# Optimization experiments

Measured on AMD Instinct MI355X. Metric: run time of the kernel, lower is better.

The kernel has to match this reference:

```python
import jax, jax.numpy as jnp
import numpy as np

N_NODES = 4096
N_EDGES = 32768
PE_DIM = 16
HIDDEN = 128


def setup_inputs() -> dict:
    key = jax.random.key(0)
    k_nodes, k_send, k_recv, k_w = jax.random.split(key, 4)
    nodes = jax.random.normal(k_nodes, (N_NODES, 8), dtype=jnp.float32)
    senders = jax.random.randint(k_send, (N_EDGES,), 0, N_NODES)
    receivers = jax.random.randint(k_recv, (N_EDGES,), 0, N_NODES)
    W = jax.random.normal(k_w, (PE_DIM, HIDDEN), dtype=jnp.float32) / np.sqrt(PE_DIM).astype(np.float32)
    b = jnp.zeros((HIDDEN,), dtype=jnp.float32)
    return {"nodes": nodes, "senders": senders, "receivers": receivers, "W": W, "b": b}


def reference(nodes, senders, receivers, W, b):
    n = nodes.shape[0]
    pe_dim = W.shape[0]
    # out-degree per node (clamped at 1, as in the original)
    ones = jnp.ones(senders.shape[0], dtype=jnp.float32)
    degree = jnp.maximum(jax.ops.segment_sum(ones, senders, num_segments=n), 1.0)
    inv_deg_e = (1.0 / degree)[senders]  # [E], per-edge 1/deg(sender)

    prob = jnp.eye(n, dtype=jnp.float32)  # [n, n] landing probabilities
    diags = []
    for _ in range(pe_dim):
        # gather sender rows, normalize, scatter-add into receiver rows
        msg = prob[senders] * inv_deg_e[:, None]           # [E, n]
        prob = jax.ops.segment_sum(msg, receivers, num_segments=n)  # [n, n]
        diags.append(jnp.diagonal(prob))                    # return probability A^k_ii
    pe = jnp.stack(diags, axis=-1)  # [n, pe_dim]
    return pe @ W + b               # [n, hidden]
```

## Files before the change

### kernel.cpp

```cpp
#include <hip/hip_runtime.h>

#define NN 4096
#define NE 32768
#define PED 16
#define HID 128
#define CW 16
#define NCHUNK 64
#define THREADS 1024
#define PASSES 4

typedef _Float16 h_t;
typedef _Float16 h8 __attribute__((ext_vector_type(8)));

__device__ __forceinline__ int xbyte(int s) {
  int g = ((s & 3) << 1) | ((s >> 2) & 1);
  return ((s >> 2) << 7) + (g << 4);
}


__global__ void count_kernel(const int* __restrict__ senders,
                             const int* __restrict__ receivers,
                             int* __restrict__ outdeg, int* __restrict__ indeg) {
  int e = blockIdx.x * blockDim.x + threadIdx.x;
  if (e < NE) {
    atomicAdd(&outdeg[senders[e]], 1);
    atomicAdd(&indeg[receivers[e]], 1);
  }
}

__global__ void sort_kernel(const int* __restrict__ indeg, const int* __restrict__ outdeg,
                            float* __restrict__ dinv,
                            int* __restrict__ rowperm, int* __restrict__ sortpos,
                            int* __restrict__ chunk_off, int* __restrict__ chunk_max) {
  __shared__ int hist[64];
  __shared__ int base[64];
  int t = threadIdx.x;
  if (t < 64) hist[t] = 0;
  __syncthreads();
  for (int r = t; r < NN; r += 256) {
    int d = indeg[r]; if (d > 63) d = 63;
    atomicAdd(&hist[d], 1);
    int od = outdeg[r]; if (od < 1) od = 1;
    dinv[r] = 1.0f / (float)od;
  }
  __syncthreads();
  if (t == 0) {
    int acc = 0;
    for (int i = 0; i < 64; ++i) { base[i] = acc; acc += hist[i]; }
  }
  __syncthreads();
  for (int r = t; r < NN; r += 256) {
    int d = indeg[r]; if (d > 63) d = 63;
    int pos = atomicAdd(&base[d], 1);
    rowperm[pos] = r;
    sortpos[r] = pos;
  }
  __syncthreads();
  if (t < NCHUNK) {
    int m = 0;
    for (int i = 0; i < 64; ++i) {
      int d = indeg[rowperm[(t << 6) + i]];
      if (d > m) m = d;
    }
    chunk_max[t] = m;
  }
  __syncthreads();
  if (t == 0) {
    int acc = 0;
    for (int c = 0; c < NCHUNK; ++c) { chunk_off[c] = acc; acc += chunk_max[c] << 6; }
    chunk_off[NCHUNK] = acc;
  }
}

__global__ void zero_tail(const int* __restrict__ chunk_off, int2* __restrict__ e2) {
  int total = chunk_off[NCHUNK];
  e2[total + threadIdx.x] = make_int2(0, 0);
}

__global__ void fill_ell(const int* __restrict__ senders, const int* __restrict__ receivers,
                         const int* __restrict__ sortpos, const int* __restrict__ chunk_off,
                         const float* __restrict__ dinv, int* __restrict__ fillc,
                         int2* __restrict__ ell) {
  int e = blockIdx.x * blockDim.x + threadIdx.x;
  if (e < NE) {
    int r = receivers[e], s = senders[e];
    int p = sortpos[r];
    int tslot = atomicAdd(&fillc[r], 1);
    int slot = chunk_off[p >> 6] + (tslot << 6) + (p & 63);
    ell[slot] = make_int2(xbyte(s), __float_as_int(dinv[s]));
  }
}

__global__ void sched_ell(const int* __restrict__ chunk_off,
                          const int* __restrict__ chunk_max,
                          const int* __restrict__ rowperm,
                          const int* __restrict__ indeg,
                          const int2* __restrict__ src, int2* __restrict__ dst) {
  int p = blockIdx.x * blockDim.x + threadIdx.x;
  int c = p >> 6, l = p & 63;
  int base = chunk_off[c], maxd = chunk_max[c];
  int d = indeg[rowperm[p]];
  if (maxd > 63) {
    for (int t = 0; t < d; ++t) dst[base + (t << 6) + l] = src[base + (t << 6) + l];
    for (int t = d; t < maxd; ++t)
      dst[base + (t << 6) + l] = make_int2(((t + l) & 7) << 4, 0);
    return;
  }
  unsigned long long occ = 0;
  int placed[8] = {0, 0, 0, 0, 0, 0, 0, 0};
  for (int t = 0; t < d; ++t) {
    int2 e = src[base + (t << 6) + l];
    int cl = (((e.x >> 4) & 7) - l) & 7;
    int slot = cl + (placed[cl]++ << 3);
    if (slot < maxd) { dst[base + (slot << 6) + l] = e; occ |= 1ull << slot; }
  }
  int placed2[8] = {0, 0, 0, 0, 0, 0, 0, 0};
  for (int t = 0; t < d; ++t) {
    int2 e = src[base + (t << 6) + l];
    int cl = (((e.x >> 4) & 7) - l) & 7;
    int slot = cl + (placed2[cl]++ << 3);
    if (slot >= maxd) {
      int f = __builtin_ctzll(~occ & ((1ull << maxd) - 1));
      dst[base + (f << 6) + l] = e;
      occ |= 1ull << f;
    }
  }
  unsigned long long rem = ~occ & ((1ull << maxd) - 1);
  while (rem) {
    int slot = __builtin_ctzll(rem);
    rem &= rem - 1;
    dst[base + (slot << 6) + l] = make_int2(((slot + l) & 7) << 4, 0);
  }
}


#define MIXL(acc, srcv) \
  asm("v_fma_mix_f32 %0, %1, %2, %0 op_sel_hi:[1,0,0]" : "+v"(acc) : "v"(srcv), "v"(w))
#define MIXH(acc, srcv) \
  asm("v_fma_mix_f32 %0, %1, %2, %0 op_sel:[1,0,0] op_sel_hi:[1,0,0]" : "+v"(acc) : "v"(srcv), "v"(w))

__global__ __launch_bounds__(THREADS, 4)
void fused_kernel(const int2* __restrict__ ell,
                  const int* __restrict__ chunk_off,
                  const int* __restrict__ chunk_max,
                  const int* __restrict__ rowperm,
                  float* __restrict__ pe) {
  __shared__ __align__(16) h_t X[NN * CW];
  char* Xb = (char*)X;
  int c0 = blockIdx.x * CW;
  int tid = threadIdx.x;
  int wave = tid >> 6, lane = tid & 63;

  for (int s = tid; s < NN; s += THREADS) {
    int dd = s - c0;
    h8 lo8, hi8;
#pragma unroll
    for (int j = 0; j < 8; ++j) {
      lo8[j] = (h_t)((dd == j) ? 1.0f : 0.0f);
      hi8[j] = (h_t)((dd == 8 + j) ? 1.0f : 0.0f);
    }
    int xb = xbyte(s);
    *reinterpret_cast<h8*>(Xb + xb) = lo8;
    *reinterpret_cast<h8*>(Xb + (xb ^ 16)) = hi8;
  }
  __syncthreads();

  for (int k = 0; k < PED; ++k) {
    h8 rlo[PASSES], rhi[PASSES];
    int rxb[PASSES];
#pragma unroll
    for (int pass = 0; pass < PASSES; ++pass) {
      int chunk = (pass << 4) + ((pass & 1) ? (15 - wave) : wave);
      int base = chunk_off[chunk];
      int maxd = chunk_max[chunk];
      int r = rowperm[(chunk << 6) + lane];
      rxb[pass] = xbyte(r);
      float a[16];
#pragma unroll
      for (int j = 0; j < 16; ++j) a[j] = 0.f;
      const int2* ep = ell + base + lane;
      int2 e0 = ep[0];
      int2 e1 = ep[64];
      int2 e2 = ep[128];
      int4 lo = *reinterpret_cast<const int4*>(Xb + e0.x);
      int4 hi = *reinterpret_cast<const int4*>(Xb + (e0.x ^ 16));
      for (int t = 0; t < maxd; ++t) {
        int2 e3 = ep[192];
        ep += 64;
        int4 nlo = *reinterpret_cast<const int4*>(Xb + e1.x);
        int4 nhi = *reinterpret_cast<const int4*>(Xb + (e1.x ^ 16));
        float w = __int_as_float(e0.y);
        MIXL(a[0], lo.x);  MIXH(a[1], lo.x);
        MIXL(a[2], lo.y);  MIXH(a[3], lo.y);
        MIXL(a[4], lo.z);  MIXH(a[5], lo.z);
        MIXL(a[6], lo.w);  MIXH(a[7], lo.w);
        MIXL(a[8], hi.x);  MIXH(a[9], hi.x);
        MIXL(a[10], hi.y); MIXH(a[11], hi.y);
        MIXL(a[12], hi.z); MIXH(a[13], hi.z);
        MIXL(a[14], hi.w); MIXH(a[15], hi.w);
        e0 = e1; e1 = e2; e2 = e3; lo = nlo; hi = nhi;
      }
      h8 plo, phi;
#pragma unroll
      for (int j = 0; j < 8; ++j) { plo[j] = (h_t)a[j]; phi[j] = (h_t)a[8 + j]; }
      rlo[pass] = plo; rhi[pass] = phi;
      int dj = r - c0;
      if (dj >= 0 && dj < CW) {
        float dv = a[0];
#pragma unroll
        for (int j = 1; j < 16; ++j) dv = (dj == j) ? a[j] : dv;
        pe[r * PED + k] = dv;
      }
    }
    __syncthreads();
#pragma unroll
    for (int pass = 0; pass < PASSES; ++pass) {
      int xb = rxb[pass];
      *reinterpret_cast<h8*>(Xb + xb) = rlo[pass];
      *reinterpret_cast<h8*>(Xb + (xb ^ 16)) = rhi[pass];
    }
    __syncthreads();
  }
}

__global__ void out_kernel(const float* __restrict__ pe, const float* __restrict__ W,
                           const float* __restrict__ bvec, float* __restrict__ out) {
  __shared__ float sW[PED * HID];
  int r = blockIdx.x;
  int h = threadIdx.x;
  for (int i = h; i < PED * HID; i += HID) sW[i] = W[i];
  __syncthreads();
  float acc = bvec[h];
  float p[PED];
#pragma unroll
  for (int kk = 0; kk < PED; ++kk) p[kk] = pe[r * PED + kk];
#pragma unroll
  for (int kk = 0; kk < PED; ++kk) acc = fmaf(p[kk], sW[kk * HID + h], acc);
  out[r * HID + h] = acc;
}

extern "C" void kernel_launch(void* const* d_in, const int* in_sizes, int n_in,
                              void* d_out, int out_size, void* d_ws, size_t ws_size,
                              hipStream_t stream) {
  const int* senders = (const int*)d_in[1];
  const int* receivers = (const int*)d_in[2];
  const float* W = (const float*)d_in[3];
  const float* bvec = (const float*)d_in[4];
  float* out = (float*)d_out;

  char* p = (char*)d_ws;
  int* outdeg = (int*)p;    p += (size_t)NN * 4;
  int* indeg = (int*)p;     p += (size_t)NN * 4;
  int* fillc = (int*)p;     p += (size_t)NN * 4;
  float* dinv = (float*)p;  p += (size_t)NN * 4;
  int* rowperm = (int*)p;   p += (size_t)NN * 4;
  int* sortpos = (int*)p;   p += (size_t)NN * 4;
  int* chunk_off = (int*)p; p += 128 * 4;
  int* chunk_max = (int*)p; p += 128 * 4;
  float* pe = (float*)p;    p += (size_t)NN * PED * 4;
  size_t ell_slots = (size_t)64 * NE + 256;
  int2* ell = (int2*)p;     p += ell_slots * sizeof(int2);
  int2* ell2 = (int2*)p;

  hipMemsetAsync(d_ws, 0, (size_t)NN * 4 * 3, stream);
  count_kernel<<<NE / 256, 256, 0, stream>>>(senders, receivers, outdeg, indeg);
  sort_kernel<<<1, 256, 0, stream>>>(indeg, outdeg, dinv, rowperm, sortpos, chunk_off, chunk_max);
  zero_tail<<<1, 256, 0, stream>>>(chunk_off, ell2);
  fill_ell<<<NE / 256, 256, 0, stream>>>(senders, receivers, sortpos, chunk_off, dinv, fillc, ell);
  sched_ell<<<NN / 256, 256, 0, stream>>>(chunk_off, chunk_max, rowperm, indeg, ell, ell2);

  fused_kernel<<<NN / CW, THREADS, 0, stream>>>(ell2, chunk_off, chunk_max, rowperm, pe);

  out_kernel<<<NN, HID, 0, stream>>>(pe, W, bvec, out);
}
```

Before: 206.2 us.

## Index X by sorted position, unroll ELL loop by two, rework bank-aware scheduling

New measurement: 246.1 us. 19.3% more time.

```diff
diff --git a/kernel.cpp b/kernel.cpp
--- a/kernel.cpp
+++ b/kernel.cpp
@@ -11,10 +11,11 @@
 
 typedef _Float16 h_t;
 typedef _Float16 h8 __attribute__((ext_vector_type(8)));
-
-__device__ __forceinline__ int xbyte(int s) {
-  int g = ((s & 3) << 1) | ((s >> 2) & 1);
-  return ((s >> 2) << 7) + (g << 4);
+typedef unsigned long long u64;
+
+__device__ __forceinline__ int xp(int p) {
+  int g = ((p & 3) << 1) | ((p >> 2) & 1);
+  return ((p >> 2) << 7) | (g << 4);
 }
 
 
@@ -31,7 +32,7 @@
 __global__ void sort_kernel(const int* __restrict__ indeg, const int* __restrict__ outdeg,
                             float* __restrict__ dinv,
                             int* __restrict__ rowperm, int* __restrict__ sortpos,
-                            int* __restrict__ chunk_off, int* __restrict__ chunk_max) {
+                            int* __restrict__ chunk_off, int* __restrict__ chunk_len) {
   __shared__ int hist[64];
   __shared__ int base[64];
   int t = threadIdx.x;
@@ -62,12 +63,12 @@
       int d = indeg[rowperm[(t << 6) + i]];
       if (d > m) m = d;
     }
-    chunk_max[t] = m;
+    chunk_len[t] = (m + 1) & ~1;
   }
   __syncthreads();
   if (t == 0) {
     int acc = 0;
-    for (int c = 0; c < NCHUNK; ++c) { chunk_off[c] = acc; acc += chunk_max[c] << 6; }
+    for (int c = 0; c < NCHUNK; ++c) { chunk_off[c] = acc; acc += chunk_len[c] << 6; }
     chunk_off[NCHUNK] = acc;
   }
 }
@@ -87,49 +88,84 @@
     int p = sortpos[r];
     int tslot = atomicAdd(&fillc[r], 1);
     int slot = chunk_off[p >> 6] + (tslot << 6) + (p & 63);
-    ell[slot] = make_int2(xbyte(s), __float_as_int(dinv[s]));
+    ell[slot] = make_int2(xp(sortpos[s]), __float_as_int(dinv[s]));
   }
 }
 
 __global__ void sched_ell(const int* __restrict__ chunk_off,
-                          const int* __restrict__ chunk_max,
+                          const int* __restrict__ chunk_len,
                           const int* __restrict__ rowperm,
                           const int* __restrict__ indeg,
                           const int2* __restrict__ src, int2* __restrict__ dst) {
-  int p = blockIdx.x * blockDim.x + threadIdx.x;
-  int c = p >> 6, l = p & 63;
-  int base = chunk_off[c], maxd = chunk_max[c];
-  int d = indeg[rowperm[p]];
-  if (maxd > 63) {
-    for (int t = 0; t < d; ++t) dst[base + (t << 6) + l] = src[base + (t << 6) + l];
-    for (int t = d; t < maxd; ++t)
-      dst[base + (t << 6) + l] = make_int2(((t + l) & 7) << 4, 0);
+  int tid = blockIdx.x * blockDim.x + threadIdx.x;
+  if (tid >= NCHUNK * 8) return;
+  int c = tid >> 3;
+  int trk = tid & 7;
+  int base = chunk_off[c];
+  int len = chunk_len[c];
+  int l0 = trk << 3;
+
+  int d[8];
+  u64 freeL[8];
+  int dmax = 0;
+#pragma unroll
+  for (int j = 0; j < 8; ++j) {
+    int dd = indeg[rowperm[(c << 6) + l0 + j]];
+    if (dd > 63) dd = 63;
+    d[j] = dd;
+    if (dd > dmax) dmax = dd;
+  }
+  if (len > 63) {
+#pragma unroll
+    for (int j = 0; j < 8; ++j) {
+      for (int t = 0; t < d[j]; ++t) dst[base + (t << 6) + l0 + j] = src[base + (t << 6) + l0 + j];
+      for (int t = d[j]; t < len; ++t) dst[base + (t << 6) + l0 + j] = make_int2(((t + j) & 7) << 4, 0);
+    }
     return;
   }
-  unsigned long long occ = 0;
-  int placed[8] = {0, 0, 0, 0, 0, 0, 0, 0};
-  for (int t = 0; t < d; ++t) {
-    int2 e = src[base + (t << 6) + l];
-    int cl = (((e.x >> 4) & 7) - l) & 7;
-    int slot = cl + (placed[cl]++ << 3);
-    if (slot < maxd) { dst[base + (slot << 6) + l] = e; occ |= 1ull << slot; }
-  }
-  int placed2[8] = {0, 0, 0, 0, 0, 0, 0, 0};
-  for (int t = 0; t < d; ++t) {
-    int2 e = src[base + (t << 6) + l];
-    int cl = (((e.x >> 4) & 7) - l) & 7;
-    int slot = cl + (placed2[cl]++ << 3);
-    if (slot >= maxd) {
-      int f = __builtin_ctzll(~occ & ((1ull << maxd) - 1));
-      dst[base + (f << 6) + l] = e;
-      occ |= 1ull << f;
-    }
-  }
-  unsigned long long rem = ~occ & ((1ull << maxd) - 1);
-  while (rem) {
-    int slot = __builtin_ctzll(rem);
-    rem &= rem - 1;
-    dst[base + (slot << 6) + l] = make_int2(((slot + l) & 7) << 4, 0);
+  u64 full = (len == 0) ? 0 : ((1ull << len) - 1);
+#pragma unroll
+  for (int j = 0; j < 8; ++j) freeL[j] = full;
+  u64 fC[8];
+#pragma unroll
+  for (int q = 0; q < 8; ++q) fC[q] = full;
+
+  for (int t = 0; t < dmax; ++t) {
+#pragma unroll
+    for (int j = 0; j < 8; ++j) {
+      if (t < d[j]) {
+        int2 e = src[base + (t << 6) + l0 + j];
+        int cls = (e.x >> 4) & 7;
+        u64 fc = 0;
+#pragma unroll
+        for (int q = 0; q < 8; ++q) fc = (q == cls) ? fC[q] : fc;
+        u64 avail = freeL[j] & fc;
+        u64 pool = avail ? avail : freeL[j];
+        u64 pick = pool & (~pool + 1);
+        int slab = __builtin_ctzll(pick);
+        freeL[j] &= ~pick;
+        if (avail) {
+#pragma unroll
+          for (int q = 0; q < 8; ++q) if (q == cls) fC[q] &= ~pick;
+        }
+        dst[base + (slab << 6) + l0 + j] = e;
+      }
+    }
+  }
+#pragma unroll
+  for (int j = 0; j < 8; ++j) {
+    u64 rem = freeL[j];
+    while (rem) {
+      u64 pick = rem & (~rem + 1);
+      rem &= rem - 1;
+      int slab = __builtin_ctzll(pick);
+      int cls = 0;
+#pragma unroll
+      for (int q = 7; q >= 0; --q) if (fC[q] & pick) cls = q;
+#pragma unroll
+      for (int q = 0; q < 8; ++q) if (q == cls) fC[q] &= ~pick;
+      dst[base + (slab << 6) + l0 + j] = make_int2(cls << 4, 0);
+    }
   }
 }
 
@@ -139,10 +175,20 @@
 #define MIXH(acc, srcv) \
   asm("v_fma_mix_f32 %0, %1, %2, %0 op_sel:[1,0,0] op_sel_hi:[1,0,0]" : "+v"(acc) : "v"(srcv), "v"(w))
 
+#define MIX16(lo, hi) \
+  MIXL(a[0], lo.x);  MIXH(a[1], lo.x);  \
+  MIXL(a[2], lo.y);  MIXH(a[3], lo.y);  \
+  MIXL(a[4], lo.z);  MIXH(a[5], lo.z);  \
+  MIXL(a[6], lo.w);  MIXH(a[7], lo.w);  \
+  MIXL(a[8], hi.x);  MIXH(a[9], hi.x);  \
+  MIXL(a[10], hi.y); MIXH(a[11], hi.y); \
+  MIXL(a[12], hi.z); MIXH(a[13], hi.z); \
+  MIXL(a[14], hi.w); MIXH(a[15], hi.w)
+
 __global__ __launch_bounds__(THREADS, 4)
 void fused_kernel(const int2* __restrict__ ell,
                   const int* __restrict__ chunk_off,
-                  const int* __restrict__ chunk_max,
+                  const int* __restrict__ chunk_len,
                   const int* __restrict__ rowperm,
                   float* __restrict__ pe) {
   __shared__ __align__(16) h_t X[NN * CW];
@@ -151,15 +197,15 @@
   int tid = threadIdx.x;
   int wave = tid >> 6, lane = tid & 63;
 
-  for (int s = tid; s < NN; s += THREADS) {
-    int dd = s - c0;
+  for (int p = tid; p < NN; p += THREADS) {
+    int dd = rowperm[p] - c0;
     h8 lo8, hi8;
 #pragma unroll
     for (int j = 0; j < 8; ++j) {
       lo8[j] = (h_t)((dd == j) ? 1.0f : 0.0f);
       hi8[j] = (h_t)((dd == 8 + j) ? 1.0f : 0.0f);
     }
-    int xb = xbyte(s);
+    int xb = xp(p);
     *reinterpret_cast<h8*>(Xb + xb) = lo8;
     *reinterpret_cast<h8*>(Xb + (xb ^ 16)) = hi8;
   }
@@ -167,14 +213,12 @@
 
   for (int k = 0; k < PED; ++k) {
     h8 rlo[PASSES], rhi[PASSES];
-    int rxb[PASSES];
 #pragma unroll
     for (int pass = 0; pass < PASSES; ++pass) {
       int chunk = (pass << 4) + ((pass & 1) ? (15 - wave) : wave);
       int base = chunk_off[chunk];
-      int maxd = chunk_max[chunk];
+      int len = chunk_len[chunk];
       int r = rowperm[(chunk << 6) + lane];
-      rxb[pass] = xbyte(r);
       float a[16];
 #pragma unroll
       for (int j = 0; j < 16; ++j) a[j] = 0.f;
@@ -182,23 +226,22 @@
       int2 e0 = ep[0];
       int2 e1 = ep[64];
       int2 e2 = ep[128];
-      int4 lo = *reinterpret_cast<const int4*>(Xb + e0.x);
-      int4 hi = *reinterpret_cast<const int4*>(Xb + (e0.x ^ 16));
-      for (int t = 0; t < maxd; ++t) {
-        int2 e3 = ep[192];
-        ep += 64;
-        int4 nlo = *reinterpret_cast<const int4*>(Xb + e1.x);
-        int4 nhi = *reinterpret_cast<const int4*>(Xb + (e1.x ^ 16));
+      int2 e3 = ep[192];
+      int4 lo0 = *reinterpret_cast<const int4*>(Xb + e0.x);
+      int4 hi0 = *reinterpret_cast<const int4*>(Xb + (e0.x ^ 16));
+      for (int t = 0; t < len; t += 2) {
+        int2 e4 = ep[256], e5 = ep[320];
+        ep += 128;
+        int4 lo1 = *reinterpret_cast<const int4*>(Xb + e1.x);
+        int4 hi1 = *reinterpret_cast<const int4*>(Xb + (e1.x ^ 16));
         float w = __int_as_float(e0.y);
-        MIXL(a[0], lo.x);  MIXH(a[1], lo.x);
-        MIXL(a[2], lo.y);  MIXH(a[3], lo.y);
-        MIXL(a[4], lo.z);  MIXH(a[5], lo.z);
-        MIXL(a[6], lo.w);  MIXH(a[7], lo.w);
-        MIXL(a[8], hi.x);  MIXH(a[9], hi.x);
-        MIXL(a[10], hi.y); MIXH(a[11], hi.y);
-        MIXL(a[12], hi.z); MIXH(a[13], hi.z);
-        MIXL(a[14], hi.w); MIXH(a[15], hi.w);
-        e0 = e1; e1 = e2; e2 = e3; lo = nlo; hi = nhi;
+        MIX16(lo0, hi0);
+        int4 nlo = *reinterpret_cast<const int4*>(Xb + e2.x);
+        int4 nhi = *reinterpret_cast<const int4*>(Xb + (e2.x ^ 16));
+        w = __int_as_float(e1.y);
+        MIX16(lo1, hi1);
+        e0 = e2; e1 = e3; e2 = e4; e3 = e5;
+        lo0 = nlo; hi0 = nhi;
       }
       h8 plo, phi;
 #pragma unroll
@@ -215,7 +258,8 @@
     __syncthreads();
 #pragma unroll
     for (int pass = 0; pass < PASSES; ++pass) {
-      int xb = rxb[pass];
+      int chunk = (pass << 4) + ((pass & 1) ? (15 - wave) : wave);
+      int xb = xp((chunk << 6) + lane);
       *reinterpret_cast<h8*>(Xb + xb) = rlo[pass];
       *reinterpret_cast<h8*>(Xb + (xb ^ 16)) = rhi[pass];
     }
@@ -256,20 +300,20 @@
   int* rowperm = (int*)p;   p += (size_t)NN * 4;
   int* sortpos = (int*)p;   p += (size_t)NN * 4;
   int* chunk_off = (int*)p; p += 128 * 4;
-  int* chunk_max = (int*)p; p += 128 * 4;
+  int* chunk_len = (int*)p; p += 128 * 4;
   float* pe = (float*)p;    p += (size_t)NN * PED * 4;
-  size_t ell_slots = (size_t)64 * NE + 256;
+  size_t ell_slots = (size_t)64 * NE + 1024;
   int2* ell = (int2*)p;     p += ell_slots * sizeof(int2);
   int2* ell2 = (int2*)p;
 
   hipMemsetAsync(d_ws, 0, (size_t)NN * 4 * 3, stream);
   count_kernel<<<NE / 256, 256, 0, stream>>>(senders, receivers, outdeg, indeg);
-  sort_kernel<<<1, 256, 0, stream>>>(indeg, outdeg, dinv, rowperm, sortpos, chunk_off, chunk_max);
-  zero_tail<<<1, 256, 0, stream>>>(chunk_off, ell2);
+  sort_kernel<<<1, 256, 0, stream>>>(indeg, outdeg, dinv, rowperm, sortpos, chunk_off, chunk_len);
+  zero_tail<<<1, 512, 0, stream>>>(chunk_off, ell2);
   fill_ell<<<NE / 256, 256, 0, stream>>>(senders, receivers, sortpos, chunk_off, dinv, fillc, ell);
-  sched_ell<<<NN / 256, 256, 0, stream>>>(chunk_off, chunk_max, rowperm, indeg, ell, ell2);
-
-  fused_kernel<<<NN / CW, THREADS, 0, stream>>>(ell2, chunk_off, chunk_max, rowperm, pe);
+  sched_ell<<<2, 256, 0, stream>>>(chunk_off, chunk_len, rowperm, indeg, ell, ell2);
+
+  fused_kernel<<<NN / CW, THREADS, 0, stream>>>(ell2, chunk_off, chunk_len, rowperm, pe);
 
   out_kernel<<<NN, HID, 0, stream>>>(pe, W, bvec, out);
 }
```
